# Optimization experiments

Hardware: AMD Instinct MI355X
Metric: run time of the kernel (lower is better)

The kernel has to match this reference:

```python
import jax, jax.numpy as jnp
import numpy as np

B, S, HID = 1, 2048, 2048
NH, NKV, D = 16, 8, 128
N_REP = NH // NKV
EPS = 1e-6
ROPE_THETA = 10000.0
N_VISION = 512  # first 512 tokens are vision, rest text


def rms_norm(x, w):
    # RMSNorm over last dim (head_dim), Qwen3 style per-head norm
    var = jnp.mean(x * x, axis=-1, keepdims=True)
    return x * jax.lax.rsqrt(var + EPS) * w


def rotate_half(x):
    half = x.shape[-1] // 2
    return jnp.concatenate([-x[..., half:], x[..., :half]], axis=-1)


def setup_inputs() -> dict:
    key = jax.random.key(0)
    ks = jax.random.split(key, 8)
    std = 0.02
    hidden_states = jax.random.normal(ks[0], (B, S, HID), jnp.float32)
    wq = jax.random.normal(ks[1], (HID, NH * D), jnp.float32) * std
    wk = jax.random.normal(ks[2], (HID, NKV * D), jnp.float32) * std
    wv = jax.random.normal(ks[3], (HID, NKV * D), jnp.float32) * std
    wo = jax.random.normal(ks[4], (NH * D, HID), jnp.float32) * std
    q_norm_w = jnp.ones((D,), jnp.float32)
    k_norm_w = jnp.ones((D,), jnp.float32)
    # RoPE tables: [1, S, D]
    pos = jnp.arange(S, dtype=jnp.float32)
    inv_freq = 1.0 / (ROPE_THETA ** (jnp.arange(0, D, 2, dtype=jnp.float32) / D))
    freqs = pos[:, None] * inv_freq[None, :]            # [S, D/2]
    emb = jnp.concatenate([freqs, freqs], axis=-1)       # [S, D]
    cos = jnp.cos(emb)[None]
    sin = jnp.sin(emb)[None]
    # additive causal mask [1,1,S,S]: 0 on/below diagonal, -1e9 above
    causal = jnp.tril(jnp.ones((S, S), jnp.bool_))
    attention_mask = jnp.where(causal, 0.0, -1e9).astype(jnp.float32)[None, None]
    # vision/text token masks [B, S]
    idx = jnp.arange(S)
    vision_mask = (idx < N_VISION)[None].astype(jnp.bool_)
    text_mask = jnp.logical_not(vision_mask)
    return {
        'hidden_states': hidden_states, 'wq': wq, 'wk': wk, 'wv': wv, 'wo': wo,
        'q_norm_w': q_norm_w, 'k_norm_w': k_norm_w, 'cos': cos, 'sin': sin,
        'attention_mask': attention_mask, 'vision_mask': vision_mask, 'text_mask': text_mask,
    }


def reference(hidden_states, wq, wk, wv, wo, q_norm_w, k_norm_w, cos, sin,
              attention_mask, vision_mask, text_mask):
    b, s, _ = hidden_states.shape
    # projections + per-head RMSNorm (q/k) -> [B, H, S, D]
    q = rms_norm((hidden_states @ wq).reshape(b, s, NH, D), q_norm_w).transpose(0, 2, 1, 3)
    k = rms_norm((hidden_states @ wk).reshape(b, s, NKV, D), k_norm_w).transpose(0, 2, 1, 3)
    v = (hidden_states @ wv).reshape(b, s, NKV, D).transpose(0, 2, 1, 3)
    # RoPE
    c = cos[:, None]  # [B,1,S,D]
    sn = sin[:, None]
    q = q * c + rotate_half(q) * sn
    k = k * c + rotate_half(k) * sn
    # GQA repeat_kv
    k = jnp.repeat(k, N_REP, axis=1)
    v = jnp.repeat(v, N_REP, axis=1)
    scaling = D ** -0.5
    scores = jnp.einsum('bhqd,bhkd->bhqk', q, k) * scaling + attention_mask
    attn = jax.nn.softmax(scores.astype(jnp.float32), axis=-1)  # [B,H,S,S]
    attn_out = jnp.einsum('bhqk,bhkd->bhqd', attn, v)
    attn_out = attn_out.transpose(0, 2, 1, 3).reshape(b, s, NH * D)
    out = attn_out @ wo  # [B,S,HID]
    # cross head scores (original runs this under no_grad on an identical eager pass)
    attn_ng = jax.lax.stop_gradient(attn)
    vm = vision_mask.astype(jnp.float32)  # [B,S]
    tm = text_mask.astype(jnp.float32)
    nv = vm.sum(-1)  # [B]
    nt = tm.sum(-1)
    v2t = jnp.einsum('bhqk,bq,bk->bh', attn_ng, vm, tm) / jnp.maximum(nv, 1.0)[:, None]
    t2v = jnp.einsum('bhqk,bq,bk->bh', attn_ng, tm, vm) / jnp.maximum(nt, 1.0)[:, None]
    valid = ((nv > 0) & (nt > 0)).astype(jnp.float32)  # [B]
    cross_scores = jnp.sum((v2t + t2v) * valid[:, None], axis=0) / jnp.maximum(valid.sum(), 1.0)
    return out, cross_scores
```

## Files before the change

### kernel.cpp

```cpp
#include <hip/hip_runtime.h>
#include <hip/hip_bf16.h>
#include <stdint.h>

typedef unsigned short u16;
typedef unsigned int u32;
typedef short s16x8 __attribute__((ext_vector_type(8)));
typedef float f32x4 __attribute__((ext_vector_type(4)));

#define S_LEN 2048
#define SCALE 0.088388347648318447f
#define LOG2E 1.4426950408889634f
#define QSCALE (SCALE * LOG2E)
#define M2 17.5f
#define NEG_BIG (-1.0e9f)
#define WAITV(N) asm volatile("s_waitcnt vmcnt(" #N ")" ::: "memory")
#define FENCE() asm volatile("" ::: "memory")
#define EXP2F(x) __builtin_amdgcn_exp2f(x)

__device__ __forceinline__ u16 f2bf(float f) {
  unsigned u = __builtin_bit_cast(unsigned, f);
  u += 0x7fffu + ((u >> 16) & 1u);
  return (u16)(u >> 16);
}
__device__ __forceinline__ float bf2f(u16 h) {
  unsigned u = ((unsigned)h) << 16;
  return __builtin_bit_cast(float, u);
}
__device__ __forceinline__ void gload16(const void* g, void* l) {
  __builtin_amdgcn_global_load_lds((const __attribute__((address_space(1))) void*)g,
                                   (__attribute__((address_space(3))) void*)l, 16, 0, 0);
}

__device__ __forceinline__ void do_transpose(const float* __restrict__ in, u16* __restrict__ out,
                                             int R, int C, int rel, int tilesx) {
  __shared__ float tile[32][33];
  int bx = (rel % tilesx) * 32, by = (rel / tilesx) * 32;
  int tx = threadIdx.x & 31, ty = threadIdx.x >> 5;
#pragma unroll
  for (int i = 0; i < 4; i++)
    tile[ty + i * 8][tx] = in[(size_t)(by + ty + i * 8) * C + bx + tx];
  __syncthreads();
#pragma unroll
  for (int i = 0; i < 4; i++)
    out[(size_t)(bx + ty + i * 8) * R + by + tx] = f2bf(tile[tx][ty + i * 8]);
}

__global__ __launch_bounds__(256) void prep_k(const float* __restrict__ hs, u16* __restrict__ hsb,
                                              const float* __restrict__ wq, const float* __restrict__ wk,
                                              const float* __restrict__ wv, const float* __restrict__ wo,
                                              u16* __restrict__ wqkvT, u16* __restrict__ woT) {
  int bid = blockIdx.x;
  if (bid < 4096) {
    int i = bid * 256 + threadIdx.x;
    float4 v = ((const float4*)hs)[i];
    ushort4 o;
    o.x = f2bf(v.x); o.y = f2bf(v.y); o.z = f2bf(v.z); o.w = f2bf(v.w);
    ((ushort4*)hsb)[i] = o;
  } else if (bid < 8192) {
    do_transpose(wq, wqkvT, 2048, 2048, bid - 4096, 64);
  } else if (bid < 10240) {
    do_transpose(wk, wqkvT + (size_t)2048 * 2048, 2048, 1024, bid - 8192, 32);
  } else if (bid < 12288) {
    do_transpose(wv, wqkvT + (size_t)3072 * 2048, 2048, 1024, bid - 10240, 32);
  } else {
    do_transpose(wo, woT, 2048, 2048, bid - 12288, 64);
  }
}

template <int BM, int F32OUT>
__global__ __launch_bounds__(BM == 256 ? 512 : 256, 2) void gemm2_k(const u16* __restrict__ A,
                                                                    const u16* __restrict__ BT,
                                                                    void* __restrict__ Cout, int N, int K) {
  constexpr int NT = (BM == 256) ? 512 : 256;
  constexpr int ALOADS = BM * 8 / NT;
  constexpr int BLOADS = 128 * 8 / NT;
  __shared__ u16 lA[2][BM * 64];
  __shared__ u16 lB[2][128 * 64];
  int tid = threadIdx.x;
  int w = tid >> 6, l = tid & 63, r = l & 15, g = l >> 4;
  int tn = blockIdx.x, tm = blockIdx.y;
  int wm = w >> 1, wn = w & 1;
  f32x4 zf = {0.f, 0.f, 0.f, 0.f};
  f32x4 acc[4][4];
#pragma unroll
  for (int mi = 0; mi < 4; mi++)
#pragma unroll
    for (int ni = 0; ni < 4; ni++) acc[mi][ni] = zf;
  int nkt = K >> 6;

  auto stage = [&](int bi, int kt) {
#pragma unroll
    for (int i = 0; i < ALOADS; i++) {
      int c = i * NT + tid;
      int row = c >> 3;
      int sb = ((c & 7) * 16) ^ ((row & 7) << 4);
      gload16(A + (size_t)(tm * BM + row) * K + kt * 64 + (sb >> 1), (char*)(&lA[bi][0]) + c * 16);
    }
#pragma unroll
    for (int i = 0; i < BLOADS; i++) {
      int c = i * NT + tid;
      int row = c >> 3;
      int sb = ((c & 7) * 16) ^ ((row & 7) << 4);
      gload16(BT + (size_t)(tn * 128 + row) * K + kt * 64 + (sb >> 1), (char*)(&lB[bi][0]) + c * 16);
    }
  };
  auto compute = [&](int bi) {
    const char* AB = (const char*)&lA[bi][0];
    const char* BB = (const char*)&lB[bi][0];
#pragma unroll
    for (int kk = 0; kk < 2; kk++) {
      s16x8 af[4], bfr[4];
#pragma unroll
      for (int mi = 0; mi < 4; mi++) {
        int row = wm * 64 + mi * 16 + r;
        af[mi] = *(const s16x8*)(AB + ((row * 128 + kk * 64 + g * 16) ^ ((r & 7) << 4)));
      }
#pragma unroll
      for (int ni = 0; ni < 4; ni++) {
        int row = wn * 64 + ni * 16 + r;
        bfr[ni] = *(const s16x8*)(BB + ((row * 128 + kk * 64 + g * 16) ^ ((r & 7) << 4)));
      }
#pragma unroll
      for (int mi = 0; mi < 4; mi++)
#pragma unroll
        for (int ni = 0; ni < 4; ni++)
          acc[mi][ni] = __builtin_amdgcn_mfma_f32_16x16x32_bf16(af[mi], bfr[ni], acc[mi][ni], 0, 0, 0);
    }
  };

  stage(0, 0);
  int cur = 0;
  for (int kt = 0; kt < nkt; ++kt) {
    if (kt + 1 < nkt) {
      stage(cur ^ 1, kt + 1);
      if (BM == 256) WAITV(6); else WAITV(8);
    } else {
      WAITV(0);
    }
    FENCE();
    __builtin_amdgcn_s_barrier();
    FENCE();
    __builtin_amdgcn_s_setprio(1);
    compute(cur);
    __builtin_amdgcn_s_setprio(0);
    FENCE();
    __builtin_amdgcn_s_barrier();
    FENCE();
    cur ^= 1;
  }

#pragma unroll
  for (int mi = 0; mi < 4; mi++) {
#pragma unroll
    for (int ni = 0; ni < 4; ni++) {
#pragma unroll
      for (int j = 0; j < 4; j++) {
        int row = tm * BM + wm * 64 + mi * 16 + g * 4 + j;
        int col = tn * 128 + wn * 64 + ni * 16 + r;
        if (F32OUT)
          ((float*)Cout)[(size_t)row * N + col] = acc[mi][ni][j];
        else
          ((u16*)Cout)[(size_t)row * N + col] = f2bf(acc[mi][ni][j]);
      }
    }
  }
}

__global__ __launch_bounds__(256) void post_k(const u16* __restrict__ qkv, const float* __restrict__ qw,
                                              const float* __restrict__ kw, const float* __restrict__ cosT,
                                              const float* __restrict__ sinT, u16* __restrict__ Qb,
                                              u16* __restrict__ Kb, u16* __restrict__ Vt,
                                              float* __restrict__ cross) {
  int bid = blockIdx.x;
  int tid = threadIdx.x;
  if (bid == 0 && tid < 16) cross[tid] = 0.f;
  if (bid < 16384) {
    int gw = bid * 4 + (tid >> 6);
    int l = tid & 63;
    int s = gw >> 5, slot = gw & 31;
    if (slot >= 24) return;
    const float* nw;
    const u16* src;
    u16* dst;
    float qs;
    if (slot < 16) {
      src = qkv + (size_t)s * 4096 + slot * 128;
      nw = qw;
      dst = Qb + ((size_t)slot * S_LEN + s) * 128;
      qs = QSCALE;
    } else {
      int hk = slot - 16;
      src = qkv + (size_t)s * 4096 + 2048 + hk * 128;
      nw = kw;
      dst = Kb + ((size_t)hk * S_LEN + s) * 128;
      qs = 1.0f;
    }
    ushort2 xv = ((const ushort2*)src)[l];
    float x0 = bf2f(xv.x), x1 = bf2f(xv.y);
    float ss = x0 * x0 + x1 * x1;
#pragma unroll
    for (int off = 1; off < 64; off <<= 1) ss += __shfl_xor(ss, off);
    float inv = rsqrtf(ss * (1.0f / 128.0f) + 1e-6f);
    int d0 = l * 2;
    float xn0 = x0 * inv * nw[d0], xn1 = x1 * inv * nw[d0 + 1];
    float p0 = __shfl_xor(xn0, 32), p1 = __shfl_xor(xn1, 32);
    float c0 = cosT[s * 128 + d0], c1 = cosT[s * 128 + d0 + 1];
    float sn0 = sinT[s * 128 + d0], sn1 = sinT[s * 128 + d0 + 1];
    float sg = (l < 32) ? -1.0f : 1.0f;
    ushort2 o;
    o.x = f2bf((xn0 * c0 + sg * p0 * sn0) * qs);
    o.y = f2bf((xn1 * c1 + sg * p1 * sn1) * qs);
    ((ushort2*)dst)[l] = o;
  } else {
    __shared__ u16 t[64][66];
    int rel = bid - 16384;
    int c0 = (rel & 15) * 64, s0 = (rel >> 4) * 64;
    int tx = tid & 63, ty = tid >> 6;
#pragma unroll
    for (int i = 0; i < 16; i++)
      t[ty + i * 4][tx] = qkv[(size_t)(s0 + ty + i * 4) * 4096 + 3072 + c0 + tx];
    __syncthreads();
#pragma unroll
    for (int i = 0; i < 16; i++)
      Vt[(size_t)(c0 + ty + i * 4) * 2048 + s0 + tx] = t[tx][ty + i * 4];
  }
}

__global__ __launch_bounds__(256, 2) void attn_k(const u16* __restrict__ Qb, const u16* __restrict__ Kb,
                                                 const u16* __restrict__ Vt, u16* __restrict__ AO,
                                                 float* __restrict__ cross) {
  __shared__ u16 Kl[2][64 * 128];
  __shared__ u16 Vl[2][128 * 64];
  __shared__ u16 Pl[4][16 * 64];
  int tid = threadIdx.x;
  int w = tid >> 6, l = tid & 63, r = l & 15, g = l >> 4;
  int bid = blockIdx.x;
  int sel = (bid >> 4) & 1;
  int idx = (bid & 15) | ((bid >> 5) << 4);
  int h = idx & 15, a = idx >> 4;
  int qb = sel ? (31 - a) : a;
  int hk = h >> 1;
  char* PlB = (char*)(&Pl[w][0]);

  int skrow = tid >> 4;
  int skoff = (tid & 15) * 16;
  int svrow = tid >> 3;
  int svoff = (tid & 7) * 16;
  auto stage = [&](int bi, int kb) {
#pragma unroll
    for (int i = 0; i < 4; i++) {
      int k = i * 16 + skrow;
      int sb = skoff ^ ((k & 7) << 4);
      gload16(Kb + (((size_t)hk * S_LEN + kb * 64 + k) << 7) + (sb >> 1),
              (char*)(&Kl[bi][0]) + (i * 256 + tid) * 16);
    }
#pragma unroll
    for (int i = 0; i < 4; i++) {
      int d = i * 32 + svrow;
      int sb = svoff ^ ((d & 7) << 4);
      gload16(Vt + (((size_t)hk * 128 + d) << 11) + kb * 64 + (sb >> 1),
              (char*)(&Vl[bi][0]) + (i * 256 + tid) * 16);
    }
  };

  int qrow = qb * 64 + w * 16 + r;
  s16x8 qf[4];
#pragma unroll
  for (int kc = 0; kc < 4; kc++)
    qf[kc] = *(const s16x8*)&Qb[((size_t)h * S_LEN + qrow) * 128 + kc * 32 + g * 8];
  f32x4 zf = {0.f, 0.f, 0.f, 0.f};
  f32x4 o_[8];
#pragma unroll
  for (int dt = 0; dt < 8; dt++) o_[dt] = zf;
  float l_ = 0.f, vs_ = 0.f;

  stage(0, 0);
  int buf = 0;
  for (int kb = 0; kb <= qb; ++kb) {
    if (kb < qb) {
      stage(buf ^ 1, kb + 1);
      WAITV(8);
    } else {
      WAITV(0);
    }
    FENCE();
    __builtin_amdgcn_s_barrier();
    FENCE();
    const char* KB = (const char*)&Kl[buf][0];
    const char* VB = (const char*)&Vl[buf][0];
    f32x4 sa[4];
    __builtin_amdgcn_s_setprio(1);
#pragma unroll
    for (int ct = 0; ct < 4; ct++) {
      sa[ct] = zf;
#pragma unroll
      for (int kc = 0; kc < 4; kc++) {
        int kbyte = (((ct * 16 + r) * 256) + kc * 64 + g * 16) ^ ((r & 7) << 4);
        sa[ct] = __builtin_amdgcn_mfma_f32_16x16x32_bf16(*(const s16x8*)(KB + kbyte), qf[kc], sa[ct], 0, 0, 0);
      }
    }
    __builtin_amdgcn_s_setprio(0);
    float sv[4][4];
    float t = 0.f;
    if (kb == qb) {
      int kb0 = kb * 64 + g * 4;
#pragma unroll
      for (int ct = 0; ct < 4; ct++)
#pragma unroll
        for (int j = 0; j < 4; j++) {
          float x = sa[ct][j] + ((kb0 + ct * 16 + j) > qrow ? NEG_BIG : 0.f);
          float p = EXP2F(x - M2);
          sv[ct][j] = p;
          t += p;
        }
    } else {
#pragma unroll
      for (int ct = 0; ct < 4; ct++)
#pragma unroll
        for (int j = 0; j < 4; j++) {
          float p = EXP2F(sa[ct][j] - M2);
          sv[ct][j] = p;
          t += p;
        }
    }
    l_ += t;
    if (kb < 8) vs_ += t;
#pragma unroll
    for (int ct = 0; ct < 4; ct++) {
      u32 lo, hi;
      asm("v_cvt_pk_bf16_f32 %0, %1, %2" : "=v"(lo) : "v"(sv[ct][0]), "v"(sv[ct][1]));
      asm("v_cvt_pk_bf16_f32 %0, %1, %2" : "=v"(hi) : "v"(sv[ct][2]), "v"(sv[ct][3]));
      uint2 pw;
      pw.x = lo;
      pw.y = hi;
      *(uint2*)(PlB + ((r * 128 + ct * 32 + g * 8) ^ ((r & 7) << 4))) = pw;
    }
    s16x8 pf[2];
#pragma unroll
    for (int kc = 0; kc < 2; kc++)
      pf[kc] = *(const s16x8*)(PlB + ((r * 128 + kc * 64 + g * 16) ^ ((r & 7) << 4)));
    __builtin_amdgcn_s_setprio(1);
#pragma unroll
    for (int dt = 0; dt < 8; dt++)
#pragma unroll
      for (int kc = 0; kc < 2; kc++) {
        int vbyte = (((dt * 16 + r) * 128) + kc * 64 + g * 16) ^ ((r & 7) << 4);
        o_[dt] = __builtin_amdgcn_mfma_f32_16x16x32_bf16(pf[kc], *(const s16x8*)(VB + vbyte), o_[dt], 0, 0, 0);
      }
    __builtin_amdgcn_s_setprio(0);
    FENCE();
    __builtin_amdgcn_s_barrier();
    FENCE();
    buf ^= 1;
  }
  l_ += __shfl_xor(l_, 16);
  l_ += __shfl_xor(l_, 32);
  vs_ += __shfl_xor(vs_, 16);
  vs_ += __shfl_xor(vs_, 32);
  float lb[4];
#pragma unroll
  for (int j = 0; j < 4; j++) lb[j] = 1.0f / __shfl(l_, g * 4 + j);
#pragma unroll
  for (int dt = 0; dt < 8; dt++)
#pragma unroll
    for (int j = 0; j < 4; j++) {
      int row = qb * 64 + w * 16 + g * 4 + j;
      int col = h * 128 + dt * 16 + r;
      AO[(size_t)row * 2048 + col] = f2bf(o_[dt][j] * lb[j]);
    }
  if (qb >= 8) {
    float acc = vs_ / l_;
#pragma unroll
    for (int off = 1; off < 64; off <<= 1) acc += __shfl_xor(acc, off);
    if (l == 0) atomicAdd(&cross[h], acc * (1.0f / (4.0f * 1536.0f)));
  }
}

extern "C" void kernel_launch(void* const* d_in, const int* in_sizes, int n_in,
                              void* d_out, int out_size, void* d_ws, size_t ws_size,
                              hipStream_t stream) {
  const float* hs = (const float*)d_in[0];
  const float* wq = (const float*)d_in[1];
  const float* wk = (const float*)d_in[2];
  const float* wv = (const float*)d_in[3];
  const float* wo = (const float*)d_in[4];
  const float* qw = (const float*)d_in[5];
  const float* kw = (const float*)d_in[6];
  const float* cosT = (const float*)d_in[7];
  const float* sinT = (const float*)d_in[8];
  float* out = (float*)d_out;
  float* cross = out + (size_t)2048 * 2048;
  char* ws = (char*)d_ws;
  u16* hsb = (u16*)ws;
  u16* wqkvT = (u16*)(ws + (8u << 20));
  u16* woT = (u16*)(ws + (24u << 20));
  u16* qkvb = (u16*)(ws + (32u << 20));
  u16* AO = hsb;
  u16* Qb = wqkvT;
  u16* Kb = (u16*)(ws + (16u << 20));
  u16* Vt = (u16*)(ws + (20u << 20));

  prep_k<<<16384, 256, 0, stream>>>(hs, hsb, wq, wk, wv, wo, wqkvT, woT);
  gemm2_k<256, 0><<<dim3(32, 8), 512, 0, stream>>>(hsb, wqkvT, qkvb, 4096, 2048);
  post_k<<<16896, 256, 0, stream>>>(qkvb, qw, kw, cosT, sinT, Qb, Kb, Vt, cross);
  attn_k<<<512, 256, 0, stream>>>(Qb, Kb, Vt, AO, cross);
  gemm2_k<128, 1><<<dim3(16, 16), 256, 0, stream>>>(AO, woT, out, 2048, 2048);
}
```

Measured before the change: 283.7 us.

## Use 64x64 transpose tiles, unify GEMM to 128x128 tiles, tree-reduce softmax sums

The weight transpose now uses 64x64 tiles with paired bf16 stores, which cuts the prep block count and widens global writes. The GEMM template drops the 256-row variant: the QKV projection runs as 128x128 tiles with 256 threads on a 32x16 grid, and the pipeline uses __syncthreads instead of the explicit vmcnt waits, barriers and priority hints. The attention softmax row sum becomes a tree reduction, which shortens the dependent add chain. Because the GEMM now relies on __syncthreads without an explicit vmcnt wait, global-to-LDS copies may not be ordered as tightly as before, and the smaller tiles give less data reuse in the QKV projection.

Measured after the change: 271.2 us. 1.05x faster.

```diff
diff --git a/kernel.cpp b/kernel.cpp
--- a/kernel.cpp
+++ b/kernel.cpp
@@ -31,18 +31,26 @@
                                    (__attribute__((address_space(3))) void*)l, 16, 0, 0);
 }
 
-__device__ __forceinline__ void do_transpose(const float* __restrict__ in, u16* __restrict__ out,
-                                             int R, int C, int rel, int tilesx) {
-  __shared__ float tile[32][33];
-  int bx = (rel % tilesx) * 32, by = (rel / tilesx) * 32;
-  int tx = threadIdx.x & 31, ty = threadIdx.x >> 5;
-#pragma unroll
-  for (int i = 0; i < 4; i++)
-    tile[ty + i * 8][tx] = in[(size_t)(by + ty + i * 8) * C + bx + tx];
+__device__ __forceinline__ void do_transpose64(const float* __restrict__ in, u16* __restrict__ out,
+                                               int R, int C, int rel, int tilesx) {
+  __shared__ float tile[64][65];
+  int bx = (rel % tilesx) * 64, by = (rel / tilesx) * 64;
+  int c = threadIdx.x & 63, rr = threadIdx.x >> 6;
+#pragma unroll
+  for (int i = 0; i < 16; i++) {
+    int r = rr + i * 4;
+    tile[c][r] = in[(size_t)(by + r) * C + bx + c];
+  }
   __syncthreads();
-#pragma unroll
-  for (int i = 0; i < 4; i++)
-    out[(size_t)(bx + ty + i * 8) * R + by + tx] = f2bf(tile[tx][ty + i * 8]);
+  int sp = threadIdx.x & 31, cc0 = threadIdx.x >> 5;
+#pragma unroll
+  for (int i = 0; i < 8; i++) {
+    int cc = cc0 + i * 8;
+    ushort2 o;
+    o.x = f2bf(tile[cc][2 * sp]);
+    o.y = f2bf(tile[cc][2 * sp + 1]);
+    *(ushort2*)&out[(size_t)(bx + cc) * R + by + 2 * sp] = o;
+  }
 }
 
 __global__ __launch_bounds__(256) void prep_k(const float* __restrict__ hs, u16* __restrict__ hsb,
@@ -56,25 +64,21 @@
     ushort4 o;
     o.x = f2bf(v.x); o.y = f2bf(v.y); o.z = f2bf(v.z); o.w = f2bf(v.w);
     ((ushort4*)hsb)[i] = o;
-  } else if (bid < 8192) {
-    do_transpose(wq, wqkvT, 2048, 2048, bid - 4096, 64);
-  } else if (bid < 10240) {
-    do_transpose(wk, wqkvT + (size_t)2048 * 2048, 2048, 1024, bid - 8192, 32);
-  } else if (bid < 12288) {
-    do_transpose(wv, wqkvT + (size_t)3072 * 2048, 2048, 1024, bid - 10240, 32);
+  } else if (bid < 5120) {
+    do_transpose64(wq, wqkvT, 2048, 2048, bid - 4096, 32);
+  } else if (bid < 5632) {
+    do_transpose64(wk, wqkvT + (size_t)2048 * 2048, 2048, 1024, bid - 5120, 16);
+  } else if (bid < 6144) {
+    do_transpose64(wv, wqkvT + (size_t)3072 * 2048, 2048, 1024, bid - 5632, 16);
   } else {
-    do_transpose(wo, woT, 2048, 2048, bid - 12288, 64);
-  }
-}
-
-template <int BM, int F32OUT>
-__global__ __launch_bounds__(BM == 256 ? 512 : 256, 2) void gemm2_k(const u16* __restrict__ A,
-                                                                    const u16* __restrict__ BT,
-                                                                    void* __restrict__ Cout, int N, int K) {
-  constexpr int NT = (BM == 256) ? 512 : 256;
-  constexpr int ALOADS = BM * 8 / NT;
-  constexpr int BLOADS = 128 * 8 / NT;
-  __shared__ u16 lA[2][BM * 64];
+    do_transpose64(wo, woT, 2048, 2048, bid - 6144, 32);
+  }
+}
+
+template <int F32OUT>
+__global__ __launch_bounds__(256, 2) void gemm_bt_k(const u16* __restrict__ A, const u16* __restrict__ BT,
+                                                    void* __restrict__ Cout, int N, int K) {
+  __shared__ u16 lA[2][128 * 64];
   __shared__ u16 lB[2][128 * 64];
   int tid = threadIdx.x;
   int w = tid >> 6, l = tid & 63, r = l & 15, g = l >> 4;
@@ -88,20 +92,16 @@
     for (int ni = 0; ni < 4; ni++) acc[mi][ni] = zf;
   int nkt = K >> 6;
 
+  int srow = tid >> 3;
+  int soff = (tid & 7) * 16;
   auto stage = [&](int bi, int kt) {
 #pragma unroll
-    for (int i = 0; i < ALOADS; i++) {
-      int c = i * NT + tid;
-      int row = c >> 3;
-      int sb = ((c & 7) * 16) ^ ((row & 7) << 4);
-      gload16(A + (size_t)(tm * BM + row) * K + kt * 64 + (sb >> 1), (char*)(&lA[bi][0]) + c * 16);
-    }
-#pragma unroll
-    for (int i = 0; i < BLOADS; i++) {
-      int c = i * NT + tid;
-      int row = c >> 3;
-      int sb = ((c & 7) * 16) ^ ((row & 7) << 4);
-      gload16(BT + (size_t)(tn * 128 + row) * K + kt * 64 + (sb >> 1), (char*)(&lB[bi][0]) + c * 16);
+    for (int i = 0; i < 4; i++) {
+      int row = i * 32 + srow;
+      int sb = soff ^ ((row & 7) << 4);
+      int L = (i * 256 + tid) * 16;
+      gload16(A + (size_t)(tm * 128 + row) * K + kt * 64 + (sb >> 1), (char*)(&lA[bi][0]) + L);
+      gload16(BT + (size_t)(tn * 128 + row) * K + kt * 64 + (sb >> 1), (char*)(&lB[bi][0]) + L);
     }
   };
   auto compute = [&](int bi) {
@@ -129,25 +129,15 @@
   };
 
   stage(0, 0);
+  __syncthreads();
   int cur = 0;
-  for (int kt = 0; kt < nkt; ++kt) {
-    if (kt + 1 < nkt) {
-      stage(cur ^ 1, kt + 1);
-      if (BM == 256) WAITV(6); else WAITV(8);
-    } else {
-      WAITV(0);
-    }
-    FENCE();
-    __builtin_amdgcn_s_barrier();
-    FENCE();
-    __builtin_amdgcn_s_setprio(1);
+  for (int kt = 0; kt + 1 < nkt; ++kt) {
+    stage(cur ^ 1, kt + 1);
     compute(cur);
-    __builtin_amdgcn_s_setprio(0);
-    FENCE();
-    __builtin_amdgcn_s_barrier();
-    FENCE();
+    __syncthreads();
     cur ^= 1;
   }
+  compute(cur);
 
 #pragma unroll
   for (int mi = 0; mi < 4; mi++) {
@@ -155,7 +145,7 @@
     for (int ni = 0; ni < 4; ni++) {
 #pragma unroll
       for (int j = 0; j < 4; j++) {
-        int row = tm * BM + wm * 64 + mi * 16 + g * 4 + j;
+        int row = tm * 128 + wm * 64 + mi * 16 + g * 4 + j;
         int col = tn * 128 + wn * 64 + ni * 16 + r;
         if (F32OUT)
           ((float*)Cout)[(size_t)row * N + col] = acc[mi][ni][j];
@@ -301,28 +291,27 @@
     }
     __builtin_amdgcn_s_setprio(0);
     float sv[4][4];
-    float t = 0.f;
+    float tct[4];
     if (kb == qb) {
       int kb0 = kb * 64 + g * 4;
 #pragma unroll
-      for (int ct = 0; ct < 4; ct++)
+      for (int ct = 0; ct < 4; ct++) {
 #pragma unroll
         for (int j = 0; j < 4; j++) {
           float x = sa[ct][j] + ((kb0 + ct * 16 + j) > qrow ? NEG_BIG : 0.f);
-          float p = EXP2F(x - M2);
-          sv[ct][j] = p;
-          t += p;
+          sv[ct][j] = EXP2F(x - M2);
         }
+        tct[ct] = (sv[ct][0] + sv[ct][1]) + (sv[ct][2] + sv[ct][3]);
+      }
     } else {
 #pragma unroll
-      for (int ct = 0; ct < 4; ct++)
-#pragma unroll
-        for (int j = 0; j < 4; j++) {
-          float p = EXP2F(sa[ct][j] - M2);
-          sv[ct][j] = p;
-          t += p;
-        }
-    }
+      for (int ct = 0; ct < 4; ct++) {
+#pragma unroll
+        for (int j = 0; j < 4; j++) sv[ct][j] = EXP2F(sa[ct][j] - M2);
+        tct[ct] = (sv[ct][0] + sv[ct][1]) + (sv[ct][2] + sv[ct][3]);
+      }
+    }
+    float t = (tct[0] + tct[1]) + (tct[2] + tct[3]);
     l_ += t;
     if (kb < 8) vs_ += t;
 #pragma unroll
@@ -400,9 +389,9 @@
   u16* Kb = (u16*)(ws + (16u << 20));
   u16* Vt = (u16*)(ws + (20u << 20));
 
-  prep_k<<<16384, 256, 0, stream>>>(hs, hsb, wq, wk, wv, wo, wqkvT, woT);
-  gemm2_k<256, 0><<<dim3(32, 8), 512, 0, stream>>>(hsb, wqkvT, qkvb, 4096, 2048);
+  prep_k<<<7168, 256, 0, stream>>>(hs, hsb, wq, wk, wv, wo, wqkvT, woT);
+  gemm_bt_k<0><<<dim3(32, 16), 256, 0, stream>>>(hsb, wqkvT, qkvb, 4096, 2048);
   post_k<<<16896, 256, 0, stream>>>(qkvb, qw, kw, cosT, sinT, Qb, Kb, Vt, cross);
   attn_k<<<512, 256, 0, stream>>>(Qb, Kb, Vt, AO, cross);
-  gemm2_k<128, 1><<<dim3(16, 16), 256, 0, stream>>>(AO, woT, out, 2048, 2048);
-}
+  gemm_bt_k<1><<<dim3(16, 16), 256, 0, stream>>>(AO, woT, out, 2048, 2048);
+}
```
